# Kernel tuning notes

Hardware: AMD Instinct MI355X
Metric: run time of the kernel (lower is better)

Reference implementation:

```python
import jax, jax.numpy as jnp
import numpy as np

MARGIN = 0.3
EPS = 1e-6  # torch TripletMarginLoss pairwise_distance eps


def setup_inputs() -> dict:
    key = jax.random.key(0)
    k1, k2 = jax.random.split(key)
    n, d = 8192, 128
    inputs = jax.random.normal(k1, (n, d), dtype=jnp.float32)
    similarity = jax.random.randint(k2, (n, n), 0, 2, dtype=jnp.int32)
    return {"inputs": inputs, "similarity": similarity}


def reference(inputs, similarity):
    # mask[i, j] = True if j is a positive of anchor i
    mask = similarity != 0                      # (n, n) bool
    maskf = mask.astype(inputs.dtype)
    counts = maskf.sum(axis=1, keepdims=True)   # (n, 1), >0 by construction
    # per-anchor center = mean of its positives (masked mean as a GEMM)
    centers = (maskf @ inputs) / counts         # (n, d)
    # dist[i, j] = ||centers[i] - inputs[j]||_2 via the expansion trick
    # (avoids materializing the (n, n, d) difference tensor of the original)
    c2 = jnp.sum(centers * centers, axis=1)[:, None]
    x2 = jnp.sum(inputs * inputs, axis=1)[None, :]
    d2 = c2 + x2 - 2.0 * (centers @ inputs.T)
    dist = jnp.sqrt(jnp.maximum(d2, 0.0))       # (n, n)
    # dist only feeds argmin in the original (indices carry no grad)
    dist = jax.lax.stop_gradient(dist)
    # hard-negative mining: argmin of dist over negatives of each anchor
    neg_idx = jnp.argmin(jnp.where(mask, jnp.inf, dist), axis=1)  # (n,)
    neg_min = inputs[neg_idx]                   # (n, d)
    # TripletMarginLoss(margin=0.3, p=2): anchor=centers, pos=inputs, neg=neg_min
    d_ap = jnp.linalg.norm(centers - inputs + EPS, axis=1)
    d_an = jnp.linalg.norm(centers - neg_min + EPS, axis=1)
    return jnp.mean(jnp.maximum(d_ap - d_an + MARGIN, 0.0))
```

## Files before the change

### kernel.cpp

```cpp
#include <hip/hip_runtime.h>
#include <stdint.h>

#define NN 8192
#define DD 128

typedef float f32x4 __attribute__((ext_vector_type(4)));
typedef short bf16x8 __attribute__((ext_vector_type(8)));

union B8 { uint32_t u[4]; bf16x8 v; };

__device__ inline uint16_t f2bf(float f) {
  uint32_t u = __builtin_bit_cast(uint32_t, f);
  uint32_t r = (u + 0x7FFFu + ((u >> 16) & 1u)) >> 16;
  return (uint16_t)r;
}

__device__ inline f32x4 mfma16(bf16x8 a, bf16x8 b, f32x4 c) {
  return __builtin_amdgcn_mfma_f32_16x16x32_bf16(a, b, c, 0, 0, 0);
}

__device__ inline void gl_lds16(const uint16_t* g, uint16_t* l) {
  __builtin_amdgcn_global_load_lds((const __attribute__((address_space(1))) void*)g,
                                   (__attribute__((address_space(3))) void*)l, 16, 0, 0);
}

__global__ __launch_bounds__(256) void k_prep(const float* __restrict__ inp,
                                              uint16_t* __restrict__ inp_bf,
                                              uint16_t* __restrict__ inpT_bf,
                                              float* __restrict__ x2p,
                                              uint32_t* __restrict__ counts,
                                              uint32_t* __restrict__ negkey,
                                              float* __restrict__ out) {
  __shared__ uint16_t ldsT[128 * 65];
  __shared__ float ldsS[256];
  const int tid = threadIdx.x;
  const int gid = blockIdx.x * 256 + tid;
  if (gid < NN) { counts[gid] = 0u; negkey[gid] = 0xFFFFFFFFu; }
  if (gid == 0) out[0] = 0.f;
  const int j0 = blockIdx.x * 64;
  const int r = tid >> 2;
  const int dseg = (tid & 3) * 32;
  float ss = 0.f;
#pragma unroll
  for (int it = 0; it < 8; ++it) {
    float4 v = *(const float4*)(inp + (size_t)(j0 + r) * DD + dseg + it * 4);
    ss += v.x * v.x + v.y * v.y + v.z * v.z + v.w * v.w;
    uint16_t b0 = f2bf(v.x), b1 = f2bf(v.y), b2 = f2bf(v.z), b3 = f2bf(v.w);
    *(ushort4*)(inp_bf + (size_t)(j0 + r) * DD + dseg + it * 4) = make_ushort4(b0, b1, b2, b3);
    int d = dseg + it * 4;
    ldsT[(d + 0) * 65 + r] = b0;
    ldsT[(d + 1) * 65 + r] = b1;
    ldsT[(d + 2) * 65 + r] = b2;
    ldsT[(d + 3) * 65 + r] = b3;
  }
  ldsS[tid] = ss;
  __syncthreads();
  if (tid < 64)
    x2p[j0 + tid] = ldsS[tid * 4] + ldsS[tid * 4 + 1] + ldsS[tid * 4 + 2] + ldsS[tid * 4 + 3] + 512.0f;
#pragma unroll
  for (int it = 0; it < 32; ++it) {
    int flat = it * 256 + tid;
    int d = flat >> 6, jl = flat & 63;
    inpT_bf[(size_t)d * NN + j0 + jl] = ldsT[d * 65 + jl];
  }
}

__global__ __launch_bounds__(256, 2) void k_bitgen(const int* __restrict__ sim,
                                                   uint32_t* __restrict__ bmT,
                                                   uint32_t* __restrict__ counts) {
  __shared__ uint32_t ldsW[64 * 64];
  const int tid = threadIdx.x, lane = tid & 63, w = tid >> 6;
  const int m0 = blockIdx.x * 64;
  const int c0 = blockIdx.y * 2048;
  int va[32], vb[32];
  {
    const int* p = sim + (size_t)(m0 + w) * NN + c0 + lane;
#pragma unroll
    for (int s = 0; s < 32; ++s) va[s] = p[s * 64];
  }
#pragma unroll 1
  for (int rr = 0; rr < 16; ++rr) {
    const int rl = rr * 4 + w;
    if (rr < 15) {
      const int* p = sim + (size_t)(m0 + rl + 4) * NN + c0 + lane;
#pragma unroll
      for (int s = 0; s < 32; ++s) vb[s] = p[s * 64];
    }
    uint32_t cnt = 0;
#pragma unroll
    for (int s = 0; s < 32; ++s) {
      unsigned long long ball = __ballot(va[s] != 0);
      cnt += (uint32_t)__popcll(ball);
      if ((lane & 31) == 0)
        ldsW[(s * 2 + (lane >> 5)) * 64 + rl] = (uint32_t)(ball >> (lane & 32));
    }
    if (lane == 0) atomicAdd(&counts[m0 + rl], cnt);
#pragma unroll
    for (int s = 0; s < 32; ++s) va[s] = vb[s];
  }
  __syncthreads();
#pragma unroll
  for (int it = 0; it < 16; ++it) {
    int idx = it * 256 + tid;
    int kw = idx >> 6, r = idx & 63;
    bmT[(size_t)((c0 >> 5) + kw) * NN + m0 + r] = ldsW[idx];
  }
}

__global__ __launch_bounds__(256, 2) void k_gemm1(const uint16_t* __restrict__ inpT,
                                                  const uint32_t* __restrict__ bmT,
                                                  float* __restrict__ part) {
  __shared__ __align__(16) uint16_t ldsB[2][128 * 64];
  const int tid = threadIdx.x, lane = tid & 63, w = tid >> 6;
  const int col = lane & 15, quad = lane >> 4;
  const int m0 = blockIdx.x * 128;
  const int kb0 = blockIdx.y * 1024;
  const int wm = (w >> 1) * 64, wn = (w & 1) * 64;
  const int swz = (col & 7) << 4;
  f32x4 acc[4][4];
  const f32x4 z = {0.f, 0.f, 0.f, 0.f};
#pragma unroll
  for (int r = 0; r < 4; ++r)
#pragma unroll
    for (int c = 0; c < 4; ++c) acc[r][c] = z;

  uint32_t mwA[8], mwB[8];
  const int srow = lane >> 3;
  const int schk = (lane & 7) ^ (srow & 7);

#define STAGE3(BUF, KB)                                                                       \
  {                                                                                           \
    _Pragma("unroll") for (int c = 0; c < 4; ++c) {                                           \
      const uint16_t* gsrc =                                                                  \
          inpT + (size_t)(w * 32 + c * 8 + srow) * NN + (KB) + (schk << 3);                   \
      gl_lds16(gsrc, &ldsB[BUF][(w * 32 + c * 8) * 64]);                                      \
    }                                                                                         \
  }

#define LDM3(MW, KB)                                                                          \
  {                                                                                           \
    _Pragma("unroll") for (int rr = 0; rr < 4; ++rr)                                          \
      _Pragma("unroll") for (int h = 0; h < 2; ++h)                                           \
        MW[rr * 2 + h] = bmT[(size_t)(((KB) >> 5) + h) * NN + m0 + wm + rr * 16 + col];       \
  }

#define COMP3(BUF, MW)                                                                        \
  {                                                                                           \
    _Pragma("unroll") for (int h = 0; h < 2; ++h) {                                           \
      B8 af[4];                                                                               \
      _Pragma("unroll") for (int rr = 0; rr < 4; ++rr) {                                      \
        uint32_t word = MW[rr * 2 + h];                                                       \
        uint32_t b = (word >> (quad * 8)) & 0xFFu;                                            \
        uint32_t s = b * 0x8001u;                                                             \
        _Pragma("unroll") for (int p = 0; p < 4; ++p)                                         \
          af[rr].u[p] = ((s >> (2 * p)) & 0x10001u) * 0x3F80u;                                \
      }                                                                                       \
      const int eoff = ((h * 64 + quad * 16) ^ swz) >> 1;                                     \
      _Pragma("unroll") for (int cc = 0; cc < 4; ++cc) {                                      \
        bf16x8 bfr = *(const bf16x8*)(&ldsB[BUF][(wn + cc * 16 + col) * 64 + eoff]);          \
        _Pragma("unroll") for (int rr = 0; rr < 4; ++rr)                                      \
          acc[rr][cc] = mfma16(af[rr].v, bfr, acc[rr][cc]);                                   \
      }                                                                                       \
    }                                                                                         \
  }

  STAGE3(0, kb0);
  LDM3(mwA, kb0);
  __syncthreads();
#pragma unroll 1
  for (int ks = 0; ks < 16; ks += 2) {
    const int kb = kb0 + ks * 64;
    STAGE3(1, kb + 64);
    LDM3(mwB, kb + 64);
    COMP3(0, mwA);
    __syncthreads();
    if (ks + 2 < 16) {
      STAGE3(0, kb + 128);
      LDM3(mwA, kb + 128);
    }
    COMP3(1, mwB);
    __syncthreads();
  }
#undef STAGE3
#undef LDM3
#undef COMP3

  float* pp = part + (size_t)blockIdx.y * NN * DD;
#pragma unroll
  for (int rr = 0; rr < 4; ++rr)
#pragma unroll
    for (int cc = 0; cc < 4; ++cc)
#pragma unroll
      for (int g = 0; g < 4; ++g)
        pp[(size_t)(m0 + wm + rr * 16 + quad * 4 + g) * DD + wn + cc * 16 + col] = acc[rr][cc][g];
}

__global__ __launch_bounds__(256) void k_reduce(const float* __restrict__ part,
                                                const uint32_t* __restrict__ counts,
                                                float* __restrict__ centers,
                                                uint16_t* __restrict__ cen_bf) {
  const int gid = blockIdx.x * 256 + threadIdx.x;
  const int idx = gid * 4;
  const int row = idx >> 7;
  const float inv = 1.0f / (float)counts[row];
  float4 v = *(const float4*)(part + idx);
#pragma unroll
  for (int s = 1; s < 8; ++s) {
    float4 u = *(const float4*)(part + (size_t)s * NN * DD + idx);
    v.x += u.x; v.y += u.y; v.z += u.z; v.w += u.w;
  }
  v.x *= inv; v.y *= inv; v.z *= inv; v.w *= inv;
  *(float4*)(centers + idx) = v;
  *(ushort4*)(cen_bf + idx) = make_ushort4(f2bf(v.x), f2bf(v.y), f2bf(v.z), f2bf(v.w));
}

__global__ __launch_bounds__(256, 2) void k_argmin(const uint16_t* __restrict__ cen_bf,
                                                   const uint16_t* __restrict__ inp_bf,
                                                   const uint32_t* __restrict__ bmT,
                                                   const float* __restrict__ x2p,
                                                   uint32_t* __restrict__ negkey) {
  __shared__ __align__(16) uint16_t ldsX[2][64 * 128];
  const int tid = threadIdx.x, lane = tid & 63, w = tid >> 6;
  const int col = lane & 15, quad = lane >> 4;
  const int i0 = blockIdx.x * 128;
  const int jbase = blockIdx.y * 1024;
  const int wi = w * 32;
  const int swz = (col & 7) << 4;

  bf16x8 af[2][4];
#pragma unroll
  for (int rr = 0; rr < 2; ++rr)
#pragma unroll
    for (int kk = 0; kk < 4; ++kk)
      af[rr][kk] = *(const bf16x8*)(cen_bf + (size_t)(i0 + wi + rr * 16 + col) * DD + kk * 32 + quad * 8);

  uint32_t best[2][4];
#pragma unroll
  for (int rr = 0; rr < 2; ++rr)
#pragma unroll
    for (int g = 0; g < 4; ++g) best[rr][g] = 0xFFFFFFFFu;

  const f32x4 z = {0.f, 0.f, 0.f, 0.f};
  const int srow = lane >> 4;

#define STAGE5(BUF, J0)                                                                       \
  {                                                                                           \
    _Pragma("unroll") for (int c = 0; c < 4; ++c) {                                           \
      const int r7 = (c * 4 + srow) & 7;                                                      \
      const uint16_t* gsrc =                                                                  \
          inp_bf + (size_t)((J0) + w * 16 + c * 4 + srow) * DD + (((lane & 15) ^ r7) << 3);   \
      gl_lds16(gsrc, &ldsX[BUF][(w * 16 + c * 4) * 128]);                                     \
    }                                                                                         \
  }

#define COMP5(BUF, J0)                                                                        \
  {                                                                                           \
    uint32_t mw[2][2][4];                                                                     \
    float xv[4];                                                                              \
    _Pragma("unroll") for (int h = 0; h < 2; ++h)                                             \
      _Pragma("unroll") for (int rr = 0; rr < 2; ++rr)                                        \
        _Pragma("unroll") for (int g = 0; g < 4; ++g)                                         \
          mw[h][rr][g] =                                                                      \
              bmT[(size_t)(((J0) >> 5) + h) * NN + i0 + wi + rr * 16 + quad * 4 + g];         \
    _Pragma("unroll") for (int cc = 0; cc < 4; ++cc) xv[cc] = x2p[(J0) + cc * 16 + col];      \
    f32x4 acc[2][4];                                                                          \
    _Pragma("unroll") for (int rr = 0; rr < 2; ++rr)                                          \
      _Pragma("unroll") for (int cc = 0; cc < 4; ++cc) acc[rr][cc] = z;                       \
    _Pragma("unroll") for (int kk = 0; kk < 4; ++kk) {                                        \
      const int eoff = ((kk * 64 + quad * 16) ^ swz) >> 1;                                    \
      _Pragma("unroll") for (int cc = 0; cc < 4; ++cc) {                                      \
        bf16x8 b = *(const bf16x8*)(&ldsX[BUF][(cc * 16 + col) * 128 + eoff]);                \
        acc[0][cc] = mfma16(af[0][kk], b, acc[0][cc]);                                        \
        acc[1][cc] = mfma16(af[1][kk], b, acc[1][cc]);                                        \
      }                                                                                       \
    }                                                                                         \
    _Pragma("unroll") for (int cc = 0; cc < 4; ++cc) {                                        \
      const int jj = cc * 16 + col;                                                           \
      const float xq = xv[cc];                                                                \
      const uint32_t jpre = (uint32_t)((J0) + jj);                                            \
      const int sh = 31 - ((cc & 1) * 16 + col);                                              \
      _Pragma("unroll") for (int rr = 0; rr < 2; ++rr)                                        \
        _Pragma("unroll") for (int g = 0; g < 4; ++g) {                                       \
          float v = fmaf(-2.0f, acc[rr][cc][g], xq);                                          \
          uint32_t u = __builtin_bit_cast(uint32_t, v);                                       \
          uint32_t key = (u & 0xFFFFE000u) | jpre;                                            \
          key |= (mw[cc >> 1][rr][g] << sh) & 0x80000000u;                                    \
          best[rr][g] = min(best[rr][g], key);                                                \
        }                                                                                     \
    }                                                                                         \
  }

  STAGE5(0, jbase);
  __syncthreads();
#pragma unroll 1
  for (int st = 0; st < 16; st += 2) {
    const int j0 = jbase + st * 64;
    STAGE5(1, j0 + 64);
    COMP5(0, j0);
    __syncthreads();
    if (st + 2 < 16) STAGE5(0, j0 + 128);
    COMP5(1, j0 + 64);
    __syncthreads();
  }
#undef STAGE5
#undef COMP5

#pragma unroll
  for (int rr = 0; rr < 2; ++rr)
#pragma unroll
    for (int g = 0; g < 4; ++g) {
      uint32_t k = best[rr][g];
#pragma unroll
      for (int d = 1; d < 16; d <<= 1) {
        uint32_t o = (uint32_t)__shfl_xor((int)k, d);
        k = min(k, o);
      }
      if (col == 0) atomicMin(&negkey[i0 + wi + rr * 16 + quad * 4 + g], k);
    }
}

__global__ __launch_bounds__(256) void k_loss(const float* __restrict__ centers,
                                              const float* __restrict__ inp,
                                              const uint32_t* __restrict__ negkey,
                                              float* __restrict__ out) {
  __shared__ float lds[4];
  const int tid = threadIdx.x, lane = tid & 63, w = tid >> 6;
  float local = 0.f;
#pragma unroll 1
  for (int a = 0; a < 4; ++a) {
    int i = blockIdx.x * 16 + w * 4 + a;
    float2 c = *(const float2*)(centers + (size_t)i * DD + lane * 2);
    float2 x = *(const float2*)(inp + (size_t)i * DD + lane * 2);
    uint32_t ni = negkey[i] & (NN - 1);
    float2 gv = *(const float2*)(inp + (size_t)ni * DD + lane * 2);
    float e0 = c.x - x.x + 1e-6f, e1 = c.y - x.y + 1e-6f;
    float f0 = c.x - gv.x + 1e-6f, f1 = c.y - gv.y + 1e-6f;
    float dap = e0 * e0 + e1 * e1;
    float dan = f0 * f0 + f1 * f1;
#pragma unroll
    for (int d = 32; d; d >>= 1) {
      dap += __shfl_down(dap, d);
      dan += __shfl_down(dan, d);
    }
    if (lane == 0) local += fmaxf(sqrtf(dap) - sqrtf(dan) + 0.3f, 0.f);
  }
  if (lane == 0) lds[w] = local;
  __syncthreads();
  if (tid == 0) atomicAdd(out, (lds[0] + lds[1] + lds[2] + lds[3]) * (1.0f / 8192.0f));
}

extern "C" void kernel_launch(void* const* d_in, const int* in_sizes, int n_in,
                              void* d_out, int out_size, void* d_ws, size_t ws_size,
                              hipStream_t stream) {
  (void)in_sizes; (void)n_in; (void)out_size; (void)ws_size;
  const float* inp = (const float*)d_in[0];
  const int* sim = (const int*)d_in[1];
  float* out = (float*)d_out;
  char* ws = (char*)d_ws;

  uint32_t* bmT     = (uint32_t*)ws;
  float* part       = (float*)(ws + (8u << 20));
  float* centers    = (float*)(ws + (40u << 20));
  uint16_t* inp_bf  = (uint16_t*)(ws + (44u << 20));
  uint16_t* inpT_bf = (uint16_t*)(ws + (46u << 20));
  uint16_t* cen_bf  = (uint16_t*)(ws + (48u << 20));
  float* x2p        = (float*)(ws + (50u << 20));
  uint32_t* counts  = (uint32_t*)(ws + (50u << 20) + 32768u);
  uint32_t* negkey  = (uint32_t*)(ws + (50u << 20) + 65536u);

  k_prep<<<128, 256, 0, stream>>>(inp, inp_bf, inpT_bf, x2p, counts, negkey, out);
  k_bitgen<<<dim3(128, 4), 256, 0, stream>>>(sim, bmT, counts);
  k_gemm1<<<dim3(64, 8), 256, 0, stream>>>(inpT_bf, bmT, part);
  k_reduce<<<1024, 256, 0, stream>>>(part, counts, centers, cen_bf);
  k_argmin<<<dim3(64, 8), 256, 0, stream>>>(cen_bf, inp_bf, bmT, x2p, negkey);
  k_loss<<<512, 256, 0, stream>>>(centers, inp, negkey, out);
}
```

Before: 443.2 us.

## Merge prep with bitgen and fold split-K reduction into GEMM tail

Prep and bitmask-generation now run as one launch, with block ranges assigned to each role. The separate reduce kernel is removed. The last GEMM block to finish each row tile, chosen through an atomic semaphore, sums the split-K partials and writes the centers. Row counts are no longer built with atomics during bitgen; they are recomputed by popcounting the bitmask in that last block. This removes two kernel launches and the launch gaps between them, at the cost of a serialized tail in the final block of each tile and extra bitmask reads.

```diff
diff --git a/kernel.cpp b/kernel.cpp
--- a/kernel.cpp
+++ b/kernel.cpp
@@ -24,93 +24,99 @@
                                    (__attribute__((address_space(3))) void*)l, 16, 0, 0);
 }
 
-__global__ __launch_bounds__(256) void k_prep(const float* __restrict__ inp,
-                                              uint16_t* __restrict__ inp_bf,
-                                              uint16_t* __restrict__ inpT_bf,
-                                              float* __restrict__ x2p,
-                                              uint32_t* __restrict__ counts,
-                                              uint32_t* __restrict__ negkey,
-                                              float* __restrict__ out) {
-  __shared__ uint16_t ldsT[128 * 65];
-  __shared__ float ldsS[256];
+__global__ __launch_bounds__(256, 2) void k_prep_bitgen(const float* __restrict__ inp,
+                                                        const int* __restrict__ sim,
+                                                        uint16_t* __restrict__ inp_bf,
+                                                        uint16_t* __restrict__ inpT_bf,
+                                                        float* __restrict__ x2p,
+                                                        uint32_t* __restrict__ bmT,
+                                                        uint32_t* __restrict__ negkey,
+                                                        uint32_t* __restrict__ sem,
+                                                        float* __restrict__ out) {
+  __shared__ uint32_t shmem[4416];
   const int tid = threadIdx.x;
-  const int gid = blockIdx.x * 256 + tid;
-  if (gid < NN) { counts[gid] = 0u; negkey[gid] = 0xFFFFFFFFu; }
-  if (gid == 0) out[0] = 0.f;
-  const int j0 = blockIdx.x * 64;
-  const int r = tid >> 2;
-  const int dseg = (tid & 3) * 32;
-  float ss = 0.f;
-#pragma unroll
-  for (int it = 0; it < 8; ++it) {
-    float4 v = *(const float4*)(inp + (size_t)(j0 + r) * DD + dseg + it * 4);
-    ss += v.x * v.x + v.y * v.y + v.z * v.z + v.w * v.w;
-    uint16_t b0 = f2bf(v.x), b1 = f2bf(v.y), b2 = f2bf(v.z), b3 = f2bf(v.w);
-    *(ushort4*)(inp_bf + (size_t)(j0 + r) * DD + dseg + it * 4) = make_ushort4(b0, b1, b2, b3);
-    int d = dseg + it * 4;
-    ldsT[(d + 0) * 65 + r] = b0;
-    ldsT[(d + 1) * 65 + r] = b1;
-    ldsT[(d + 2) * 65 + r] = b2;
-    ldsT[(d + 3) * 65 + r] = b3;
-  }
-  ldsS[tid] = ss;
-  __syncthreads();
-  if (tid < 64)
-    x2p[j0 + tid] = ldsS[tid * 4] + ldsS[tid * 4 + 1] + ldsS[tid * 4 + 2] + ldsS[tid * 4 + 3] + 512.0f;
-#pragma unroll
-  for (int it = 0; it < 32; ++it) {
-    int flat = it * 256 + tid;
-    int d = flat >> 6, jl = flat & 63;
-    inpT_bf[(size_t)d * NN + j0 + jl] = ldsT[d * 65 + jl];
-  }
-}
-
-__global__ __launch_bounds__(256, 2) void k_bitgen(const int* __restrict__ sim,
-                                                   uint32_t* __restrict__ bmT,
-                                                   uint32_t* __restrict__ counts) {
-  __shared__ uint32_t ldsW[64 * 64];
-  const int tid = threadIdx.x, lane = tid & 63, w = tid >> 6;
-  const int m0 = blockIdx.x * 64;
-  const int c0 = blockIdx.y * 2048;
-  int va[32], vb[32];
-  {
-    const int* p = sim + (size_t)(m0 + w) * NN + c0 + lane;
-#pragma unroll
-    for (int s = 0; s < 32; ++s) va[s] = p[s * 64];
-  }
-#pragma unroll 1
-  for (int rr = 0; rr < 16; ++rr) {
-    const int rl = rr * 4 + w;
-    if (rr < 15) {
-      const int* p = sim + (size_t)(m0 + rl + 4) * NN + c0 + lane;
-#pragma unroll
-      for (int s = 0; s < 32; ++s) vb[s] = p[s * 64];
-    }
-    uint32_t cnt = 0;
-#pragma unroll
-    for (int s = 0; s < 32; ++s) {
-      unsigned long long ball = __ballot(va[s] != 0);
-      cnt += (uint32_t)__popcll(ball);
-      if ((lane & 31) == 0)
-        ldsW[(s * 2 + (lane >> 5)) * 64 + rl] = (uint32_t)(ball >> (lane & 32));
-    }
-    if (lane == 0) atomicAdd(&counts[m0 + rl], cnt);
-#pragma unroll
-    for (int s = 0; s < 32; ++s) va[s] = vb[s];
-  }
-  __syncthreads();
-#pragma unroll
-  for (int it = 0; it < 16; ++it) {
-    int idx = it * 256 + tid;
-    int kw = idx >> 6, r = idx & 63;
-    bmT[(size_t)((c0 >> 5) + kw) * NN + m0 + r] = ldsW[idx];
+  const int bid = blockIdx.x;
+  if (bid < 128) {
+    uint16_t* ldsT = (uint16_t*)shmem;
+    float* ldsS = (float*)(shmem + 4160);
+    const int gid = bid * 256 + tid;
+    if (gid < NN) negkey[gid] = 0xFFFFFFFFu;
+    if (gid < 64) sem[gid] = 0u;
+    if (gid == 0) out[0] = 0.f;
+    const int j0 = bid * 64;
+    const int r = tid >> 2;
+    const int dseg = (tid & 3) * 32;
+    float ss = 0.f;
+#pragma unroll
+    for (int it = 0; it < 8; ++it) {
+      float4 v = *(const float4*)(inp + (size_t)(j0 + r) * DD + dseg + it * 4);
+      ss += v.x * v.x + v.y * v.y + v.z * v.z + v.w * v.w;
+      uint16_t b0 = f2bf(v.x), b1 = f2bf(v.y), b2 = f2bf(v.z), b3 = f2bf(v.w);
+      *(ushort4*)(inp_bf + (size_t)(j0 + r) * DD + dseg + it * 4) = make_ushort4(b0, b1, b2, b3);
+      int d = dseg + it * 4;
+      ldsT[(d + 0) * 65 + r] = b0;
+      ldsT[(d + 1) * 65 + r] = b1;
+      ldsT[(d + 2) * 65 + r] = b2;
+      ldsT[(d + 3) * 65 + r] = b3;
+    }
+    ldsS[tid] = ss;
+    __syncthreads();
+    if (tid < 64)
+      x2p[j0 + tid] = ldsS[tid * 4] + ldsS[tid * 4 + 1] + ldsS[tid * 4 + 2] + ldsS[tid * 4 + 3] + 512.0f;
+#pragma unroll
+    for (int it = 0; it < 32; ++it) {
+      int flat = it * 256 + tid;
+      int d = flat >> 6, jl = flat & 63;
+      inpT_bf[(size_t)d * NN + j0 + jl] = ldsT[d * 65 + jl];
+    }
+  } else {
+    uint32_t* ldsW = shmem;
+    const int bx = bid - 128;
+    const int lane = tid & 63, w = tid >> 6;
+    const int m0 = (bx & 127) * 64;
+    const int c0 = (bx >> 7) * 2048;
+    int va[32], vb[32];
+    {
+      const int* p = sim + (size_t)(m0 + w) * NN + c0 + lane;
+#pragma unroll
+      for (int s = 0; s < 32; ++s) va[s] = p[s * 64];
+    }
+#pragma unroll 1
+    for (int rr = 0; rr < 16; ++rr) {
+      const int rl = rr * 4 + w;
+      if (rr < 15) {
+        const int* p = sim + (size_t)(m0 + rl + 4) * NN + c0 + lane;
+#pragma unroll
+        for (int s = 0; s < 32; ++s) vb[s] = p[s * 64];
+      }
+#pragma unroll
+      for (int s = 0; s < 32; ++s) {
+        unsigned long long ball = __ballot(va[s] != 0);
+        if ((lane & 31) == 0)
+          ldsW[(s * 2 + (lane >> 5)) * 64 + rl] = (uint32_t)(ball >> (lane & 32));
+      }
+#pragma unroll
+      for (int s = 0; s < 32; ++s) va[s] = vb[s];
+    }
+    __syncthreads();
+#pragma unroll
+    for (int it = 0; it < 16; ++it) {
+      int idx = it * 256 + tid;
+      int kw = idx >> 6, r = idx & 63;
+      bmT[(size_t)((c0 >> 5) + kw) * NN + m0 + r] = ldsW[idx];
+    }
   }
 }
 
 __global__ __launch_bounds__(256, 2) void k_gemm1(const uint16_t* __restrict__ inpT,
                                                   const uint32_t* __restrict__ bmT,
-                                                  float* __restrict__ part) {
+                                                  float* __restrict__ part,
+                                                  uint32_t* __restrict__ sem,
+                                                  float* __restrict__ centers,
+                                                  uint16_t* __restrict__ cen_bf) {
   __shared__ __align__(16) uint16_t ldsB[2][128 * 64];
+  __shared__ float sInv[128];
+  __shared__ uint32_t s_done;
   const int tid = threadIdx.x, lane = tid & 63, w = tid >> 6;
   const int col = lane & 15, quad = lane >> 4;
   const int m0 = blockIdx.x * 128;
@@ -193,25 +199,39 @@
 #pragma unroll
       for (int g = 0; g < 4; ++g)
         pp[(size_t)(m0 + wm + rr * 16 + quad * 4 + g) * DD + wn + cc * 16 + col] = acc[rr][cc][g];
-}
-
-__global__ __launch_bounds__(256) void k_reduce(const float* __restrict__ part,
-                                                const uint32_t* __restrict__ counts,
-                                                float* __restrict__ centers,
-                                                uint16_t* __restrict__ cen_bf) {
-  const int gid = blockIdx.x * 256 + threadIdx.x;
-  const int idx = gid * 4;
-  const int row = idx >> 7;
-  const float inv = 1.0f / (float)counts[row];
-  float4 v = *(const float4*)(part + idx);
-#pragma unroll
-  for (int s = 1; s < 8; ++s) {
-    float4 u = *(const float4*)(part + (size_t)s * NN * DD + idx);
-    v.x += u.x; v.y += u.y; v.z += u.z; v.w += u.w;
-  }
-  v.x *= inv; v.y *= inv; v.z *= inv; v.w *= inv;
-  *(float4*)(centers + idx) = v;
-  *(ushort4*)(cen_bf + idx) = make_ushort4(f2bf(v.x), f2bf(v.y), f2bf(v.z), f2bf(v.w));
+
+  __threadfence();
+  __syncthreads();
+  if (tid == 0) s_done = atomicAdd(&sem[blockIdx.x], 1u);
+  __syncthreads();
+  if (s_done != 7u) return;
+  __threadfence();
+
+  if (tid < 128) {
+    uint32_t cnt = 0;
+#pragma unroll 4
+    for (int kw = 0; kw < 256; ++kw) cnt += __popc(bmT[(size_t)kw * NN + m0 + tid]);
+    sInv[tid] = 1.0f / (float)cnt;
+  }
+  __syncthreads();
+
+#pragma unroll 1
+  for (int it = 0; it < 16; ++it) {
+    const int f4 = it * 256 + tid;
+    const int row = f4 >> 5;
+    const int c4 = (f4 & 31) * 4;
+    const size_t idx = (size_t)(m0 + row) * DD + c4;
+    float4 v = *(const float4*)(part + idx);
+#pragma unroll
+    for (int s = 1; s < 8; ++s) {
+      float4 u = *(const float4*)(part + (size_t)s * NN * DD + idx);
+      v.x += u.x; v.y += u.y; v.z += u.z; v.w += u.w;
+    }
+    const float inv = sInv[row];
+    v.x *= inv; v.y *= inv; v.z *= inv; v.w *= inv;
+    *(float4*)(centers + idx) = v;
+    *(ushort4*)(cen_bf + idx) = make_ushort4(f2bf(v.x), f2bf(v.y), f2bf(v.z), f2bf(v.w));
+  }
 }
 
 __global__ __launch_bounds__(256, 2) void k_argmin(const uint16_t* __restrict__ cen_bf,
@@ -365,13 +385,11 @@
   uint16_t* inpT_bf = (uint16_t*)(ws + (46u << 20));
   uint16_t* cen_bf  = (uint16_t*)(ws + (48u << 20));
   float* x2p        = (float*)(ws + (50u << 20));
-  uint32_t* counts  = (uint32_t*)(ws + (50u << 20) + 32768u);
+  uint32_t* sem     = (uint32_t*)(ws + (50u << 20) + 32768u);
   uint32_t* negkey  = (uint32_t*)(ws + (50u << 20) + 65536u);
 
-  k_prep<<<128, 256, 0, stream>>>(inp, inp_bf, inpT_bf, x2p, counts, negkey, out);
-  k_bitgen<<<dim3(128, 4), 256, 0, stream>>>(sim, bmT, counts);
-  k_gemm1<<<dim3(64, 8), 256, 0, stream>>>(inpT_bf, bmT, part);
-  k_reduce<<<1024, 256, 0, stream>>>(part, counts, centers, cen_bf);
+  k_prep_bitgen<<<640, 256, 0, stream>>>(inp, sim, inp_bf, inpT_bf, x2p, bmT, negkey, sem, out);
+  k_gemm1<<<dim3(64, 8), 256, 0, stream>>>(inpT_bf, bmT, part, sem, centers, cen_bf);
   k_argmin<<<dim3(64, 8), 256, 0, stream>>>(cen_bf, inp_bf, bmT, x2p, negkey);
   k_loss<<<512, 256, 0, stream>>>(centers, inp, negkey, out);
 }
```

Result: slower. 518.6 us (+17.0%).
